# Kernel tuning notes

Hardware: AMD Instinct MI355X
Metric: run time of the kernel (lower is better)

Reference implementation:

```python
import jax, jax.numpy as jnp
import numpy as np

B, N = 32, 1024
NUM = B * N
DIMS = [(1, 128, 8), (128, 128, 8), (128, 64, 16), (64, 64, 16), (64, 32, 1)]  # (cin, cout, heads)

def _edges():
    # bidirectional chain per batch element, offset by N per graph (as in torch forward)
    a = np.arange(N - 1)
    offs = (np.arange(B) * N)[:, None]
    src = np.concatenate([(a[None] + offs).ravel(), (a[None] + 1 + offs).ravel()])
    dst = np.concatenate([(a[None] + 1 + offs).ravel(), (a[None] + offs).ravel()])
    return jnp.asarray(src, jnp.int32), jnp.asarray(dst, jnp.int32)

def _conv(x, src, dst, Wm, bm, Ws, bs, att):
    # PyG GeneralConv: directed msg, additive attention, aggr='add', head-mean, + lin_self
    h, cout = att.shape
    m = (x @ Wm + bm)[src].reshape(-1, h, cout)          # [E, H, C] edge messages
    m = jnp.where(m > 0, m, 0.01 * m)                    # F.leaky_relu default slope 0.01
    alpha = jnp.einsum('ehc,hc->eh', m, att)             # [E, H] attention logits
    amax = jax.ops.segment_max(alpha, dst, num_segments=NUM)
    ex = jnp.exp(alpha - amax[dst])
    den = jax.ops.segment_sum(ex, dst, num_segments=NUM)
    w = ex / (den[dst] + 1e-16)                          # segment softmax over incoming edges
    agg = jax.ops.segment_sum(m * w[:, :, None], dst, num_segments=NUM)  # [NUM, H, C]
    return agg.mean(axis=1) + x @ Ws + bs                # head mean + self loop linear

def _forward(nodes, params, Wc, bc):
    src, dst = _edges()
    x = nodes.reshape(NUM, 1)
    for i, p in enumerate(params):
        x = _conv(x, src, dst, *p)
        if i < 4:
            x = jax.nn.elu(x)                            # Dropout(0.4) identity at eval
    out = x.reshape(B, N, -1)[:, -1, :]                  # last node per graph -> [B, 32]
    return out @ Wc + bc, out

def setup_inputs():
    key = jax.random.key(0)
    ks = jax.random.split(key, 20)
    inp = {"nodes": jax.random.normal(ks[0], (B, N), dtype=jnp.float32)}
    i = 1
    for l, (cin, cout, h) in enumerate(DIMS, 1):
        s = float(1.0 / np.sqrt(cin))
        inp["Wm%d" % l] = jax.random.uniform(ks[i], (cin, h * cout), jnp.float32, -s, s); i += 1
        inp["bm%d" % l] = jnp.zeros((h * cout,), jnp.float32)
        inp["Ws%d" % l] = jax.random.uniform(ks[i], (cin, cout), jnp.float32, -s, s); i += 1
        inp["bs%d" % l] = jnp.zeros((cout,), jnp.float32)
        inp["att%d" % l] = jax.random.normal(ks[i], (h, cout), jnp.float32) * 0.1; i += 1
    inp["Wc"] = jax.random.normal(ks[i], (32, 1), jnp.float32) * 0.1
    inp["bc"] = jnp.zeros((1,), jnp.float32)
    return inp

def reference(nodes, Wm1, bm1, Ws1, bs1, att1, Wm2, bm2, Ws2, bs2, att2, Wm3, bm3, Ws3, bs3, att3, Wm4, bm4, Ws4, bs4, att4, Wm5, bm5, Ws5, bs5, att5, Wc, bc):
    params = [(Wm1, bm1, Ws1, bs1, att1), (Wm2, bm2, Ws2, bs2, att2), (Wm3, bm3, Ws3, bs3, att3), (Wm4, bm4, Ws4, bs4, att4), (Wm5, bm5, Ws5, bs5, att5)]
    return _forward(nodes, params, Wc, bc)
```

## Files before the change

kernel.cpp:

```cpp
#include <hip/hip_runtime.h>

#define BATCH 32
#define NLEN  1024
#define NUMV  (BATCH * NLEN)

typedef __attribute__((ext_vector_type(8))) short short8;
typedef __attribute__((ext_vector_type(4))) float f32x4;

__device__ inline unsigned short rne_bf16(float x) {
    union { float f; unsigned u; } a; a.f = x;
    return (unsigned short)((a.u + 0x7FFFu + ((a.u >> 16) & 1u)) >> 16);
}
__device__ inline void bsplit(float x, unsigned short& h, unsigned short& l) {
    union { float f; unsigned u; } a; a.f = x;
    unsigned hb = (a.u + 0x7FFFu + ((a.u >> 16) & 1u)) & 0xFFFF0000u;
    h = (unsigned short)(hb >> 16);
    union { unsigned u; float f; } hf; hf.u = hb;
    l = rne_bf16(x - hf.f);
}
__device__ inline float bf16_to_f(unsigned short v) {
    union { unsigned u; float f; } a; a.u = ((unsigned)v) << 16; return a.f;
}

template<int CIN, int COUT, int H>
__device__ void pack_layer(const float* __restrict__ Wm, const float* __restrict__ Ws,
                           unsigned short* __restrict__ out, int t0, int nthr)
{
    constexpr int HC = H * COUT;
    constexpr int KC = ((CIN + 31) & ~31) / 32;
    constexpr int NT = (HC + COUT) / 16;
    const int total = NT * KC * 1024;
    for (int f = t0; f < total; f += nthr) {
        int j  = f & 7;
        int c  = (f >> 3) & 15;
        int g  = (f >> 7) & 3;
        int hl = (f >> 9) & 1;
        int r2 = f >> 10;
        int kc = r2 % KC, nt = r2 / KC;
        int k = kc * 32 + g * 8 + j, col = nt * 16 + c;
        float v = 0.f;
        if (k < CIN) v = (col < HC) ? Wm[k * HC + col] : Ws[k * COUT + (col - HC)];
        unsigned short h, l; bsplit(v, h, l);
        out[f] = hl ? l : h;
    }
}

__global__ void pack_all(const float* Wm1, const float* Ws1, const float* Wm2, const float* Ws2,
                         const float* Wm3, const float* Ws3, const float* Wm4, const float* Ws4,
                         unsigned short* p1, unsigned short* p2, unsigned short* p3, unsigned short* p4)
{
    int t = blockIdx.x * 256 + threadIdx.x;
    int n = gridDim.x * 256;
    pack_layer<1, 128, 8>(Wm1, Ws1, p1, t, n);
    pack_layer<128, 128, 8>(Wm2, Ws2, p2, t, n);
    pack_layer<128, 64, 16>(Wm3, Ws3, p3, t, n);
    pack_layer<64, 64, 16>(Wm4, Ws4, p4, t, n);
}

template<int CIN, int COUT, int H, bool MPACK>
__global__ __launch_bounds__(256, 3)
void conv_reg(const float* __restrict__ x, const unsigned short* __restrict__ pw,
              const float* __restrict__ bm, const float* __restrict__ bs,
              const float* __restrict__ att, float* __restrict__ y)
{
    constexpr int HC = H * COUT;
    static_assert(HC == 1024, "");
    constexpr int KC   = ((CIN + 31) & ~31) / 32;
    constexpr int HT   = COUT / 16;
    constexpr int MT   = HC / 16;
    constexpr int NTOT = MT + HT;
    constexpr int NCH  = KC * 128;
    constexpr int CHPT = (NCH + 255) / 256;
    constexpr int ROWSB = 56;
    constexpr int TPG  = (NLEN + ROWSB - 1) / ROWSB;
    constexpr float invH = 1.0f / H;

    const int tid  = threadIdx.x;
    const int lane = tid & 63;
    const int w    = tid >> 6;
    const int r    = lane & 15;
    const int gg   = lane >> 4;
    const int g    = blockIdx.x / TPG;
    const int n0   = (blockIdx.x % TPG) * ROWSB;
    const size_t gstart = (size_t)g * NLEN;

    __shared__ alignas(16) unsigned short bufs[2][KC * 1024];

    short8 a_hi[KC], a_lo[KC];
    {
        const int na = n0 - 1 + w * 14 + r;
        const bool av = (na >= 0) && (na < NLEN);
        const float* xrow = x + (gstart + (size_t)(av ? na : 0)) * CIN;
        #pragma unroll
        for (int kc = 0; kc < KC; kc++) {
            float vals[8];
            if constexpr (CIN % 32 == 0) {
                if (av) {
                    f32x4 v0 = *(const f32x4*)(xrow + kc * 32 + gg * 8);
                    f32x4 v1 = *(const f32x4*)(xrow + kc * 32 + gg * 8 + 4);
                    vals[0]=v0[0]; vals[1]=v0[1]; vals[2]=v0[2]; vals[3]=v0[3];
                    vals[4]=v1[0]; vals[5]=v1[1]; vals[6]=v1[2]; vals[7]=v1[3];
                } else {
                    #pragma unroll
                    for (int jj = 0; jj < 8; jj++) vals[jj] = 0.f;
                }
            } else {
                #pragma unroll
                for (int jj = 0; jj < 8; jj++) {
                    int k = kc * 32 + gg * 8 + jj;
                    vals[jj] = (av && k < CIN) ? xrow[k] : 0.f;
                }
            }
            union { short8 v; unsigned short u[8]; } hu, lu;
            #pragma unroll
            for (int jj = 0; jj < 8; jj++) bsplit(vals[jj], hu.u[jj], lu.u[jj]);
            a_hi[kc] = hu.v; a_lo[kc] = lu.v;
        }
    }

    float out[HT][4];
    #pragma unroll
    for (int q = 0; q < HT; q++)
        #pragma unroll
        for (int e = 0; e < 4; e++) out[q][e] = 0.f;

    float    mf[MPACK ? 1 : HT][4];
    unsigned mpk[MPACK ? HT : 1][2];

    {
        const f32x4* ps = (const f32x4*)pw;
        f32x4 sreg[CHPT];
        #pragma unroll
        for (int i = 0; i < CHPT; i++) { int idx = tid + i * 256; if (idx < NCH) sreg[i] = ps[idx]; }
        #pragma unroll
        for (int i = 0; i < CHPT; i++) { int idx = tid + i * 256; if (idx < NCH) *(f32x4*)&bufs[0][idx * 8] = sreg[i]; }
    }
    __syncthreads();

    const int boff = gg * 128 + r * 8;

    for (int h = 0; h < H; h++) {
        float p[4] = {0.f, 0.f, 0.f, 0.f};
        #pragma unroll
        for (int q = 0; q < HT; q++) {
            const int nt  = h * HT + q;
            const int cur = nt & 1;
            const int ntn = nt + 1;
            const bool doStage = (ntn < NTOT);
            f32x4 sreg[CHPT];
            if (doStage) {
                const f32x4* ps = (const f32x4*)pw + (size_t)ntn * NCH;
                #pragma unroll
                for (int i = 0; i < CHPT; i++) { int idx = tid + i * 256; if (idx < NCH) sreg[i] = ps[idx]; }
            }
            const int col  = nt * 16 + r;
            const float bmv  = bm[col];
            const float attv = att[col];
            short8 bh[KC], bl[KC];
            #pragma unroll
            for (int kc = 0; kc < KC; kc++) {
                bh[kc] = *(const short8*)&bufs[cur][(kc * 2 + 0) * 512 + boff];
                bl[kc] = *(const short8*)&bufs[cur][(kc * 2 + 1) * 512 + boff];
            }
            f32x4 acc = {bmv, bmv, bmv, bmv};
            #pragma unroll
            for (int kc = 0; kc < KC; kc++) {
                acc = __builtin_amdgcn_mfma_f32_16x16x32_bf16(a_hi[kc], bh[kc], acc, 0, 0, 0);
                acc = __builtin_amdgcn_mfma_f32_16x16x32_bf16(a_hi[kc], bl[kc], acc, 0, 0, 0);
                acc = __builtin_amdgcn_mfma_f32_16x16x32_bf16(a_lo[kc], bh[kc], acc, 0, 0, 0);
            }
            float vv[4];
            #pragma unroll
            for (int e = 0; e < 4; e++) {
                float v = acc[e];
                v = v > 0.f ? v : 0.01f * v;
                vv[e] = v;
                p[e] += v * attv;
            }
            if constexpr (MPACK) {
                mpk[q][0] = ((unsigned)rne_bf16(vv[1]) << 16) | rne_bf16(vv[0]);
                mpk[q][1] = ((unsigned)rne_bf16(vv[3]) << 16) | rne_bf16(vv[2]);
            } else {
                #pragma unroll
                for (int e = 0; e < 4; e++) mf[q][e] = vv[e];
            }
            if (doStage) {
                const int nb = ntn & 1;
                #pragma unroll
                for (int i = 0; i < CHPT; i++) { int idx = tid + i * 256; if (idx < NCH) *(f32x4*)&bufs[nb][idx * 8] = sreg[i]; }
            }
            __syncthreads();
        }
        #pragma unroll
        for (int e = 0; e < 4; e++) {
            float v = p[e];
            v += __shfl_xor(v, 1, 64);
            v += __shfl_xor(v, 2, 64);
            v += __shfl_xor(v, 4, 64);
            v += __shfl_xor(v, 8, 64);
            p[e] = v;
        }
        {
            const int jbase = w * 14;
            float a3u = __shfl_up(p[3], 16, 64);
            float a0d = __shfl_down(p[0], 16, 64);
            float wpv[4], wnv[4];
            #pragma unroll
            for (int e = 0; e < 4; e++) {
                const int jr = gg * 4 + e;
                const int nl = n0 - 1 + jbase + jr;
                const bool hp = nl >= 1;
                const bool hn = nl < NLEN - 1;
                float ap = (e > 0) ? p[e - 1] : a3u;
                float an = (e < 3) ? p[e + 1] : a0d;
                float apx = hp ? ap : -1e30f;
                float anx = hn ? an : -1e30f;
                float mx = fmaxf(apx, anx);
                float ep = hp ? __expf(ap - mx) : 0.f;
                float en = hn ? __expf(an - mx) : 0.f;
                float inv = 1.f / (ep + en + 1e-16f);
                wpv[e] = ep * inv; wnv[e] = en * inv;
            }
            #pragma unroll
            for (int q = 0; q < HT; q++) {
                float v0, v1, v2, v3;
                if constexpr (MPACK) {
                    v0 = bf16_to_f((unsigned short)(mpk[q][0] & 0xffff));
                    v1 = bf16_to_f((unsigned short)(mpk[q][0] >> 16));
                    v2 = bf16_to_f((unsigned short)(mpk[q][1] & 0xffff));
                    v3 = bf16_to_f((unsigned short)(mpk[q][1] >> 16));
                } else {
                    v0 = mf[q][0]; v1 = mf[q][1]; v2 = mf[q][2]; v3 = mf[q][3];
                }
                float m3u = __shfl_up(v3, 16, 64);
                float m0d = __shfl_down(v0, 16, 64);
                float mvals[4] = {v0, v1, v2, v3};
                #pragma unroll
                for (int e = 0; e < 4; e++) {
                    float mprev = (e > 0) ? mvals[e - 1] : m3u;
                    float mnext = (e < 3) ? mvals[e + 1] : m0d;
                    out[q][e] += wpv[e] * mprev + wnv[e] * mnext;
                }
            }
        }
    }

    #pragma unroll
    for (int q2 = 0; q2 < HT; q2++) {
        const int nt  = MT + q2;
        const int cur = nt & 1;
        const int ntn = nt + 1;
        const bool doStage = (ntn < NTOT);
        f32x4 sreg[CHPT];
        if (doStage) {
            const f32x4* ps = (const f32x4*)pw + (size_t)ntn * NCH;
            #pragma unroll
            for (int i = 0; i < CHPT; i++) { int idx = tid + i * 256; if (idx < NCH) sreg[i] = ps[idx]; }
        }
        const int c2  = q2 * 16 + r;
        const float bsv = bs[c2];
        short8 bh[KC], bl[KC];
        #pragma unroll
        for (int kc = 0; kc < KC; kc++) {
            bh[kc] = *(const short8*)&bufs[cur][(kc * 2 + 0) * 512 + boff];
            bl[kc] = *(const short8*)&bufs[cur][(kc * 2 + 1) * 512 + boff];
        }
        f32x4 acc = {bsv, bsv, bsv, bsv};
        #pragma unroll
        for (int kc = 0; kc < KC; kc++) {
            acc = __builtin_amdgcn_mfma_f32_16x16x32_bf16(a_hi[kc], bh[kc], acc, 0, 0, 0);
            acc = __builtin_amdgcn_mfma_f32_16x16x32_bf16(a_hi[kc], bl[kc], acc, 0, 0, 0);
            acc = __builtin_amdgcn_mfma_f32_16x16x32_bf16(a_lo[kc], bh[kc], acc, 0, 0, 0);
        }
        const int jbase = w * 14;
        #pragma unroll
        for (int e = 0; e < 4; e++) {
            const int jr = gg * 4 + e;
            const int nl = n0 - 1 + jbase + jr;
            float v = out[q2][e] * invH + acc[e];
            v = v > 0.f ? v : __expf(v) - 1.f;
            if (jr >= 1 && jr <= 14 && nl < NLEN)
                y[(gstart + nl) * COUT + c2] = v;
        }
        if (doStage) {
            const int nb = ntn & 1;
            #pragma unroll
            for (int i = 0; i < CHPT; i++) { int idx = tid + i * 256; if (idx < NCH) *(f32x4*)&bufs[nb][idx * 8] = sreg[i]; }
        }
        __syncthreads();
    }
}

__global__ void final_head(const float* __restrict__ x4,
                           const float* __restrict__ Wm,
                           const float* __restrict__ bm,
                           const float* __restrict__ Ws,
                           const float* __restrict__ bs,
                           const float* __restrict__ Wc,
                           const float* __restrict__ bc,
                           float* __restrict__ out)
{
    int g = blockIdx.x;
    int c = threadIdx.x;
    const float* xu = &x4[((long)g * NLEN + NLEN - 2) * 64];
    const float* xv = xu + 64;
    float o = 0.f;
    if (c < 32) {
        float m = bm[c];
        float s = bs[c];
        for (int k = 0; k < 64; k++) {
            m = fmaf(xu[k], Wm[k * 32 + c], m);
            s = fmaf(xv[k], Ws[k * 32 + c], s);
        }
        m = m > 0.f ? m : 0.01f * m;
        o = m + s;
        out[32 + g * 32 + c] = o;
    }
    float tsum = (c < 32) ? o * Wc[c] : 0.f;
    #pragma unroll
    for (int sft = 16; sft > 0; sft >>= 1)
        tsum += __shfl_xor(tsum, sft, 64);
    if (c == 0) out[g] = tsum + bc[0];
}

extern "C" void kernel_launch(void* const* d_in, const int* in_sizes, int n_in,
                              void* d_out, int out_size, void* d_ws, size_t ws_size,
                              hipStream_t stream)
{
    const float* nodes = (const float*)d_in[0];
    auto L = [&](int l, int k) { return (const float*)d_in[1 + (l - 1) * 5 + k]; };

    float* xb0 = (float*)d_ws;
    float* xb1 = xb0 + (size_t)NUMV * 128;
    unsigned short* p1 = (unsigned short*)(xb1 + (size_t)NUMV * 128);
    unsigned short* p2 = p1 + 72 * 1024;
    unsigned short* p3 = p2 + 72 * 4096;
    unsigned short* p4 = p3 + 68 * 4096;

    pack_all<<<dim3(512), dim3(256), 0, stream>>>(
        L(1,0), L(1,2), L(2,0), L(2,2), L(3,0), L(3,2), L(4,0), L(4,2), p1, p2, p3, p4);

    constexpr int TPG = (NLEN + 55) / 56;
    dim3 grid(BATCH * TPG);
    dim3 blk(256);

    conv_reg<1,   128, 8,  false><<<grid, blk, 0, stream>>>(nodes, p1, L(1,1), L(1,3), L(1,4), xb0);
    conv_reg<128, 128, 8,  true ><<<grid, blk, 0, stream>>>(xb0,   p2, L(2,1), L(2,3), L(2,4), xb1);
    conv_reg<128, 64,  16, false><<<grid, blk, 0, stream>>>(xb1,   p3, L(3,1), L(3,3), L(3,4), xb0);
    conv_reg<64,  64,  16, false><<<grid, blk, 0, stream>>>(xb0,   p4, L(4,1), L(4,3), L(4,4), xb1);

    final_head<<<dim3(BATCH), dim3(64), 0, stream>>>(
        xb1, L(5,0), L(5,1), L(5,2), L(5,3),
        (const float*)d_in[26], (const float*)d_in[27], (float*)d_out);
}
```

Baseline: 341.7 us.

## Halve conv block size, stage bias/att in LDS, split MFMA accumulator chains

Blocks shrink from 256 to 128 threads, each covering 28 rows instead of 56, so the grid doubles and occupancy is raised. Per-column bias and attention values are preloaded into shared memory as float2 pairs, replacing per-tile global loads. The first weight-tile staging now overlaps with the A-fragment load. The three dependent MFMA chains (hi*hi, hi*lo, lo*hi) get separate accumulators to break the serial dependency. In exchange, each block loads the same weight tiles for fewer rows, so redundant weight traffic and the halo-row overhead double.

```diff
diff --git a/kernel.cpp b/kernel.cpp
--- a/kernel.cpp
+++ b/kernel.cpp
@@ -58,7 +58,7 @@
 }
 
 template<int CIN, int COUT, int H, bool MPACK>
-__global__ __launch_bounds__(256, 3)
+__global__ __launch_bounds__(128, 4)
 void conv_reg(const float* __restrict__ x, const unsigned short* __restrict__ pw,
               const float* __restrict__ bm, const float* __restrict__ bs,
               const float* __restrict__ att, float* __restrict__ y)
@@ -70,9 +70,11 @@
     constexpr int MT   = HC / 16;
     constexpr int NTOT = MT + HT;
     constexpr int NCH  = KC * 128;
-    constexpr int CHPT = (NCH + 255) / 256;
-    constexpr int ROWSB = 56;
+    constexpr int NTHR = 128;
+    constexpr int CHPT = (NCH + NTHR - 1) / NTHR;
+    constexpr int ROWSB = 28;
     constexpr int TPG  = (NLEN + ROWSB - 1) / ROWSB;
+    constexpr int PL   = HC + COUT;
     constexpr float invH = 1.0f / H;
 
     const int tid  = threadIdx.x;
@@ -85,6 +87,20 @@
     const size_t gstart = (size_t)g * NLEN;
 
     __shared__ alignas(16) unsigned short bufs[2][KC * 1024];
+    __shared__ alignas(8) float pl[PL * 2];
+
+    for (int i = tid; i < PL; i += NTHR) {
+        if (i < HC) { pl[2 * i] = bm[i]; pl[2 * i + 1] = att[i]; }
+        else        { pl[2 * i] = bs[i - HC]; pl[2 * i + 1] = 0.f; }
+    }
+    {
+        const f32x4* ps = (const f32x4*)pw;
+        f32x4 sreg[CHPT];
+        #pragma unroll
+        for (int i = 0; i < CHPT; i++) { int idx = tid + i * NTHR; if (idx < NCH) sreg[i] = ps[idx]; }
+        #pragma unroll
+        for (int i = 0; i < CHPT; i++) { int idx = tid + i * NTHR; if (idx < NCH) *(f32x4*)&bufs[0][idx * 8] = sreg[i]; }
+    }
 
     short8 a_hi[KC], a_lo[KC];
     {
@@ -127,14 +143,6 @@
     float    mf[MPACK ? 1 : HT][4];
     unsigned mpk[MPACK ? HT : 1][2];
 
-    {
-        const f32x4* ps = (const f32x4*)pw;
-        f32x4 sreg[CHPT];
-        #pragma unroll
-        for (int i = 0; i < CHPT; i++) { int idx = tid + i * 256; if (idx < NCH) sreg[i] = ps[idx]; }
-        #pragma unroll
-        for (int i = 0; i < CHPT; i++) { int idx = tid + i * 256; if (idx < NCH) *(f32x4*)&bufs[0][idx * 8] = sreg[i]; }
-    }
     __syncthreads();
 
     const int boff = gg * 128 + r * 8;
@@ -151,31 +159,32 @@
             if (doStage) {
                 const f32x4* ps = (const f32x4*)pw + (size_t)ntn * NCH;
                 #pragma unroll
-                for (int i = 0; i < CHPT; i++) { int idx = tid + i * 256; if (idx < NCH) sreg[i] = ps[idx]; }
-            }
-            const int col  = nt * 16 + r;
-            const float bmv  = bm[col];
-            const float attv = att[col];
+                for (int i = 0; i < CHPT; i++) { int idx = tid + i * NTHR; if (idx < NCH) sreg[i] = ps[idx]; }
+            }
+            const int col = nt * 16 + r;
+            const float2 pv = *(const float2*)&pl[col * 2];
             short8 bh[KC], bl[KC];
             #pragma unroll
             for (int kc = 0; kc < KC; kc++) {
                 bh[kc] = *(const short8*)&bufs[cur][(kc * 2 + 0) * 512 + boff];
                 bl[kc] = *(const short8*)&bufs[cur][(kc * 2 + 1) * 512 + boff];
             }
-            f32x4 acc = {bmv, bmv, bmv, bmv};
+            f32x4 acc0 = {pv.x, pv.x, pv.x, pv.x};
+            f32x4 acc1 = {0.f, 0.f, 0.f, 0.f};
+            f32x4 acc2 = {0.f, 0.f, 0.f, 0.f};
             #pragma unroll
             for (int kc = 0; kc < KC; kc++) {
-                acc = __builtin_amdgcn_mfma_f32_16x16x32_bf16(a_hi[kc], bh[kc], acc, 0, 0, 0);
-                acc = __builtin_amdgcn_mfma_f32_16x16x32_bf16(a_hi[kc], bl[kc], acc, 0, 0, 0);
-                acc = __builtin_amdgcn_mfma_f32_16x16x32_bf16(a_lo[kc], bh[kc], acc, 0, 0, 0);
+                acc0 = __builtin_amdgcn_mfma_f32_16x16x32_bf16(a_hi[kc], bh[kc], acc0, 0, 0, 0);
+                acc1 = __builtin_amdgcn_mfma_f32_16x16x32_bf16(a_hi[kc], bl[kc], acc1, 0, 0, 0);
+                acc2 = __builtin_amdgcn_mfma_f32_16x16x32_bf16(a_lo[kc], bh[kc], acc2, 0, 0, 0);
             }
             float vv[4];
             #pragma unroll
             for (int e = 0; e < 4; e++) {
-                float v = acc[e];
+                float v = acc0[e] + acc1[e] + acc2[e];
                 v = v > 0.f ? v : 0.01f * v;
                 vv[e] = v;
-                p[e] += v * attv;
+                p[e] += v * pv.y;
             }
             if constexpr (MPACK) {
                 mpk[q][0] = ((unsigned)rne_bf16(vv[1]) << 16) | rne_bf16(vv[0]);
@@ -187,7 +196,7 @@
             if (doStage) {
                 const int nb = ntn & 1;
                 #pragma unroll
-                for (int i = 0; i < CHPT; i++) { int idx = tid + i * 256; if (idx < NCH) *(f32x4*)&bufs[nb][idx * 8] = sreg[i]; }
+                for (int i = 0; i < CHPT; i++) { int idx = tid + i * NTHR; if (idx < NCH) *(f32x4*)&bufs[nb][idx * 8] = sreg[i]; }
             }
             __syncthreads();
         }
@@ -255,29 +264,31 @@
         if (doStage) {
             const f32x4* ps = (const f32x4*)pw + (size_t)ntn * NCH;
             #pragma unroll
-            for (int i = 0; i < CHPT; i++) { int idx = tid + i * 256; if (idx < NCH) sreg[i] = ps[idx]; }
+            for (int i = 0; i < CHPT; i++) { int idx = tid + i * NTHR; if (idx < NCH) sreg[i] = ps[idx]; }
         }
         const int c2  = q2 * 16 + r;
-        const float bsv = bs[c2];
+        const float bsv = pl[(HC + c2) * 2];
         short8 bh[KC], bl[KC];
         #pragma unroll
         for (int kc = 0; kc < KC; kc++) {
             bh[kc] = *(const short8*)&bufs[cur][(kc * 2 + 0) * 512 + boff];
             bl[kc] = *(const short8*)&bufs[cur][(kc * 2 + 1) * 512 + boff];
         }
-        f32x4 acc = {bsv, bsv, bsv, bsv};
+        f32x4 acc0 = {bsv, bsv, bsv, bsv};
+        f32x4 acc1 = {0.f, 0.f, 0.f, 0.f};
+        f32x4 acc2 = {0.f, 0.f, 0.f, 0.f};
         #pragma unroll
         for (int kc = 0; kc < KC; kc++) {
-            acc = __builtin_amdgcn_mfma_f32_16x16x32_bf16(a_hi[kc], bh[kc], acc, 0, 0, 0);
-            acc = __builtin_amdgcn_mfma_f32_16x16x32_bf16(a_hi[kc], bl[kc], acc, 0, 0, 0);
-            acc = __builtin_amdgcn_mfma_f32_16x16x32_bf16(a_lo[kc], bh[kc], acc, 0, 0, 0);
+            acc0 = __builtin_amdgcn_mfma_f32_16x16x32_bf16(a_hi[kc], bh[kc], acc0, 0, 0, 0);
+            acc1 = __builtin_amdgcn_mfma_f32_16x16x32_bf16(a_hi[kc], bl[kc], acc1, 0, 0, 0);
+            acc2 = __builtin_amdgcn_mfma_f32_16x16x32_bf16(a_lo[kc], bh[kc], acc2, 0, 0, 0);
         }
         const int jbase = w * 14;
         #pragma unroll
         for (int e = 0; e < 4; e++) {
             const int jr = gg * 4 + e;
             const int nl = n0 - 1 + jbase + jr;
-            float v = out[q2][e] * invH + acc[e];
+            float v = out[q2][e] * invH + (acc0[e] + acc1[e] + acc2[e]);
             v = v > 0.f ? v : __expf(v) - 1.f;
             if (jr >= 1 && jr <= 14 && nl < NLEN)
                 y[(gstart + nl) * COUT + c2] = v;
@@ -285,7 +296,7 @@
         if (doStage) {
             const int nb = ntn & 1;
             #pragma unroll
-            for (int i = 0; i < CHPT; i++) { int idx = tid + i * 256; if (idx < NCH) *(f32x4*)&bufs[nb][idx * 8] = sreg[i]; }
+            for (int i = 0; i < CHPT; i++) { int idx = tid + i * NTHR; if (idx < NCH) *(f32x4*)&bufs[nb][idx * 8] = sreg[i]; }
         }
         __syncthreads();
     }
@@ -340,9 +351,9 @@
     pack_all<<<dim3(512), dim3(256), 0, stream>>>(
         L(1,0), L(1,2), L(2,0), L(2,2), L(3,0), L(3,2), L(4,0), L(4,2), p1, p2, p3, p4);
 
-    constexpr int TPG = (NLEN + 55) / 56;
+    constexpr int TPG = (NLEN + 27) / 28;
     dim3 grid(BATCH * TPG);
-    dim3 blk(256);
+    dim3 blk(128);
 
     conv_reg<1,   128, 8,  false><<<grid, blk, 0, stream>>>(nodes, p1, L(1,1), L(1,3), L(1,4), xb0);
     conv_reg<128, 128, 8,  true ><<<grid, blk, 0, stream>>>(xb0,   p2, L(2,1), L(2,3), L(2,4), xb1);
```

After: 633.1 us. +85.3%, slower.
